# Optimization experiments

Measured on AMD Instinct MI355X. Metric: run time of the kernel, lower is better.

Reference implementation:

```python
import jax, jax.numpy as jnp
import numpy as np

B, L, D, H, A, NLAYERS, P = 16, 512, 768, 4, 100, 2, 3
DK = A // H  # 25
EPS = 1e-6


def setup_inputs() -> dict:
    key = jax.random.key(0)
    ks = jax.random.split(key, 20)
    s = 0.02
    return {
        "sequence_output": jax.random.normal(ks[0], (B, L, D), jnp.float32),
        "syntax_matrix": jax.random.normal(ks[1], (B, H, L, L), jnp.float32),
        # LayerNorm params
        "ln_a": jnp.ones((D,), jnp.float32),
        "ln_b": jnp.zeros((D,), jnp.float32),
        # Wxx: bert_dim -> attdim
        "Wxx_w": jax.random.normal(ks[2], (A, D), jnp.float32) * s,
        "Wxx_b": jnp.zeros((A,), jnp.float32),
        # attention q/k projections (attdim -> attdim)
        "q_w": jax.random.normal(ks[3], (A, A), jnp.float32) * s,
        "q_b": jnp.zeros((A,), jnp.float32),
        "k_w": jax.random.normal(ks[4], (A, A), jnp.float32) * s,
        "k_b": jnp.zeros((A,), jnp.float32),
        # W: attdim -> attdim
        "W_w": jax.random.normal(ks[5], (A, A), jnp.float32) * s,
        "W_b": jnp.zeros((A,), jnp.float32),
        # Wx: (H + 2*attdim) -> H
        "Wx_w": jax.random.normal(ks[6], (H, H + 2 * A), jnp.float32) * s,
        "Wx_b": jnp.zeros((H,), jnp.float32),
        # aggregate_W: attdim*(layers+1) -> attdim
        "agg_w": jax.random.normal(ks[7], (A, A * (NLAYERS + 1)), jnp.float32) * s,
        "agg_b": jnp.zeros((A,), jnp.float32),
        # classifier: 100 -> polarities_dim
        "cls_w": jax.random.normal(ks[8], (P, A), jnp.float32) * s,
        "cls_b": jnp.zeros((P,), jnp.float32),
        # masks (ints)
        "mask_ids": jnp.ones((B, L), jnp.int32),
        "src_mask": jnp.ones((B, L), jnp.int32),
    }


def reference(sequence_output, syntax_matrix, ln_a, ln_b, Wxx_w, Wxx_b,
              q_w, q_b, k_w, k_b, W_w, W_b, Wx_w, Wx_b,
              agg_w, agg_b, cls_w, cls_b, mask_ids, src_mask):
    # custom LayerNorm: torch.std is unbiased (ddof=1)
    mean = sequence_output.mean(-1, keepdims=True)
    std = jnp.std(sequence_output, axis=-1, ddof=1, keepdims=True)
    seq = ln_a * (sequence_output - mean) / (std + EPS) + ln_b

    # Wxx projection to attdim (dropout = identity in eval)
    x = seq @ Wxx_w.T + Wxx_b  # [B, L, A]

    # multi-head attention producing adjacency [B, H, L, L]
    q = (x @ q_w.T + q_b).reshape(B, L, H, DK).transpose(0, 2, 1, 3)
    k = (x @ k_w.T + k_b).reshape(B, L, H, DK).transpose(0, 2, 1, 3)
    scores = jnp.einsum('bhid,bhjd->bhij', q, k) / jnp.sqrt(jnp.float32(DK))
    key_mask = src_mask[:, None, None, :]  # [B,1,1,L]
    scores = jnp.where(key_mask == 0, jnp.float32(-1e9), scores)
    scores = scores + syntax_matrix
    adj = jax.nn.softmax(scores, axis=-1)  # [B, H, L, L]

    # split Wx into its adjacency / node-j / node-i blocks so the [B,L,L,H+2A]
    # concat tensor is never materialized (edge MLP is linear => decomposable)
    Aw = Wx_w[:, :H]            # [H, H]
    B1 = Wx_w[:, H:H + A]       # [H, A] applied to x[b, j]
    B2 = Wx_w[:, H + A:]        # [H, A] applied to x[b, i]

    x_g = x
    layer_list = [x]
    for i in range(NLAYERS):
        # Ax = mean over heads of adj_h @ x  (x identical per head)
        Ax = jnp.einsum('bhij,bjd->bid', adj, x_g) / H
        x_g = jax.nn.relu(Ax @ W_w.T + W_b)  # [B, L, A]
        layer_list.append(x_g)
        # edge update: edge[b,g,i,j] = sum_h Aw[g,h]*adj[b,h,i,j]
        e_adj = jnp.einsum('bhij,gh->bgij', adj, Aw)  # [B, H, L, L]
        u = jnp.einsum('bjd,gd->bgj', x_g, B1)        # node1 (index j)
        v = jnp.einsum('bid,gd->bgi', x_g, B2)        # node2 (index i)
        adj = e_adj + u[:, :, None, :] + v[:, :, :, None] + Wx_b[None, :, None, None]

    feats = jnp.concatenate(layer_list, axis=-1)          # [B, L, A*(NLAYERS+1)]
    node = jax.nn.relu(feats @ agg_w.T + agg_b)           # [B, L, A]

    valid_len = jnp.clip(mask_ids.sum(axis=1), 1, None).astype(node.dtype)[:, None]
    pooled = node.sum(axis=1) / valid_len                 # [B, A]
    logits = pooled @ cls_w.T + cls_b                     # [B, P]
    return logits
```

## Files before the change

### kernel.cpp

```cpp
#include <hip/hip_runtime.h>

#define B_ 16
#define L_ 512
#define D_ 768
#define H_ 4
#define A_ 100
#define DK_ 25
#define P_ 3
#define XP_ 128

__global__ __launch_bounds__(256) void k_prep(
    const float* __restrict__ Wxx_w, const float* __restrict__ agg_w,
    const float* __restrict__ q_w, const float* __restrict__ k_w,
    const float* __restrict__ W_w,
    float* __restrict__ wT, float* __restrict__ aggT,
    float* __restrict__ qkT, float* __restrict__ WT)
{
    int idx = blockIdx.x * 256 + threadIdx.x;
    if (idx < 98304) {
        const int d = idx >> 7, a = idx & 127;
        wT[idx] = (a < A_) ? Wxx_w[(size_t)a * D_ + d] : 0.f;
        return;
    }
    idx -= 98304;
    if (idx < 38400) {
        const int n = idx & 127, k = (idx >> 7) % A_, c = idx / (128 * A_);
        aggT[idx] = (n < A_) ? agg_w[(size_t)n * (3 * A_) + c * A_ + k] : 0.f;
        return;
    }
    idx -= 38400;
    if (idx < 25600) {
        const int n = idx & 255, k = idx >> 8;
        const int half = n >> 7, a = n & 127;
        const float* w = half ? k_w : q_w;
        qkT[idx] = (a < A_) ? w[(size_t)a * A_ + k] : 0.f;
        return;
    }
    idx -= 25600;
    if (idx < 12800) {
        const int n = idx & 127, k = idx >> 7;
        WT[idx] = (n < A_) ? W_w[(size_t)n * A_ + k] : 0.f;
    }
}

__global__ __launch_bounds__(256) void k_lnx(
    const float* __restrict__ seq, const float* __restrict__ ln_a, const float* __restrict__ ln_b,
    const float* __restrict__ wT, const float* __restrict__ Wxx_b, float* __restrict__ xp)
{
    __shared__ float ss[32][36];
    __shared__ float ws[32][128];
    __shared__ float mean_s[32], rd_s[32];
    const int tid = threadIdx.x;
    const int row0 = blockIdx.x * 32;
    const int wv = tid >> 6, lane = tid & 63;

    for (int rr = 0; rr < 8; ++rr) {
        const int r = wv * 8 + rr;
        const float4* src = (const float4*)(seq + (size_t)(row0 + r) * D_);
        float4 a = src[lane], b = src[lane + 64], c = src[lane + 128];
        float s = a.x + a.y + a.z + a.w + b.x + b.y + b.z + b.w + c.x + c.y + c.z + c.w;
        #pragma unroll
        for (int o = 32; o; o >>= 1) s += __shfl_xor(s, o);
        const float m = s * (1.0f / 768.0f);
        float q = (a.x-m)*(a.x-m) + (a.y-m)*(a.y-m) + (a.z-m)*(a.z-m) + (a.w-m)*(a.w-m)
                + (b.x-m)*(b.x-m) + (b.y-m)*(b.y-m) + (b.z-m)*(b.z-m) + (b.w-m)*(b.w-m)
                + (c.x-m)*(c.x-m) + (c.y-m)*(c.y-m) + (c.z-m)*(c.z-m) + (c.w-m)*(c.w-m);
        #pragma unroll
        for (int o = 32; o; o >>= 1) q += __shfl_xor(q, o);
        if (lane == 0) {
            mean_s[r] = m;
            rd_s[r] = 1.0f / (sqrtf(q * (1.0f / 767.0f)) + 1e-6f);
        }
    }
    __syncthreads();

    const int c4 = tid & 31, rg = tid >> 5;
    float4 acc[4];
    #pragma unroll
    for (int i = 0; i < 4; ++i) { acc[i].x = acc[i].y = acc[i].z = acc[i].w = 0.f; }

    for (int kc = 0; kc < 24; ++kc) {
        {
            const int r = tid >> 3, k4 = tid & 7;
            float4 v = *(const float4*)(seq + (size_t)(row0 + r) * D_ + kc * 32 + k4 * 4);
            float4 la = ((const float4*)ln_a)[kc * 8 + k4];
            float4 lb = ((const float4*)ln_b)[kc * 8 + k4];
            const float m = mean_s[r], rd = rd_s[r];
            float4 o;
            o.x = la.x * ((v.x - m) * rd) + lb.x;
            o.y = la.y * ((v.y - m) * rd) + lb.y;
            o.z = la.z * ((v.z - m) * rd) + lb.z;
            o.w = la.w * ((v.w - m) * rd) + lb.w;
            *(float4*)&ss[r][k4 * 4] = o;
        }
        #pragma unroll
        for (int t = 0; t < 4; ++t) {
            const int idx = tid + t * 256;
            const int k = idx >> 5, cc = idx & 31;
            *(float4*)&ws[k][cc * 4] = *(const float4*)(wT + (size_t)(kc * 32 + k) * 128 + cc * 4);
        }
        __syncthreads();
        #pragma unroll 2
        for (int k = 0; k < 32; k += 4) {
            float4 sv[4];
            #pragma unroll
            for (int i = 0; i < 4; ++i) sv[i] = *(float4*)&ss[rg * 4 + i][k];
            #pragma unroll
            for (int j = 0; j < 4; ++j) {
                float4 w4 = *(float4*)&ws[k + j][c4 * 4];
                #pragma unroll
                for (int i = 0; i < 4; ++i) {
                    const float sj = ((float*)&sv[i])[j];
                    acc[i].x += sj * w4.x; acc[i].y += sj * w4.y;
                    acc[i].z += sj * w4.z; acc[i].w += sj * w4.w;
                }
            }
        }
        __syncthreads();
    }

    float4 bias = {0.f, 0.f, 0.f, 0.f};
    if (c4 < 25) bias = ((const float4*)Wxx_b)[c4];
    #pragma unroll
    for (int i = 0; i < 4; ++i) {
        float4 o;
        o.x = acc[i].x + bias.x; o.y = acc[i].y + bias.y;
        o.z = acc[i].z + bias.z; o.w = acc[i].w + bias.w;
        *(float4*)(xp + (size_t)(row0 + rg * 4 + i) * XP_ + c4 * 4) = o;
    }
}

__global__ __launch_bounds__(256) void k_qkg(
    const float* __restrict__ xp, const float* __restrict__ qkT,
    const float* __restrict__ q_b, const float* __restrict__ k_b,
    float* __restrict__ qt, float* __restrict__ kt)
{
    __shared__ float ss[32][104];
    __shared__ float ws[A_][128];
    const int tid = threadIdx.x;
    const int row0 = blockIdx.x * 32;
    const int half = blockIdx.y;
    const int c4 = tid & 31, rg = tid >> 5;

    for (int idx = tid; idx < 32 * 25; idx += 256) {
        const int r = idx / 25, k4 = idx % 25;
        *(float4*)&ss[r][k4 * 4] = *(const float4*)(xp + (size_t)(row0 + r) * XP_ + k4 * 4);
    }
    for (int idx = tid; idx < A_ * 32; idx += 256) {
        const int k = idx >> 5, cc = idx & 31;
        *(float4*)&ws[k][cc * 4] = *(const float4*)(qkT + (size_t)k * 256 + half * 128 + cc * 4);
    }
    __syncthreads();

    float4 acc[4];
    #pragma unroll
    for (int i = 0; i < 4; ++i) { acc[i].x = acc[i].y = acc[i].z = acc[i].w = 0.f; }
    #pragma unroll 5
    for (int k = 0; k < A_; k += 4) {
        float4 sv[4];
        #pragma unroll
        for (int i = 0; i < 4; ++i) sv[i] = *(float4*)&ss[rg * 4 + i][k];
        #pragma unroll
        for (int j = 0; j < 4; ++j) {
            float4 w4 = *(float4*)&ws[k + j][c4 * 4];
            #pragma unroll
            for (int i = 0; i < 4; ++i) {
                const float sj = ((float*)&sv[i])[j];
                acc[i].x += sj * w4.x; acc[i].y += sj * w4.y;
                acc[i].z += sj * w4.z; acc[i].w += sj * w4.w;
            }
        }
    }

    if (c4 < 25) {
        const float4 bias = ((const float4*)(half ? k_b : q_b))[c4];
        float* dst = half ? kt : qt;
        #pragma unroll
        for (int i = 0; i < 4; ++i) {
            float4 o;
            o.x = acc[i].x + bias.x; o.y = acc[i].y + bias.y;
            o.z = acc[i].z + bias.z; o.w = acc[i].w + bias.w;
            *(float4*)(dst + (size_t)(row0 + rg * 4 + i) * A_ + c4 * 4) = o;
        }
    }
}

#define NI_ 8
#define SCS 516
__global__ __launch_bounds__(256) void k_attn(
    const float* __restrict__ qt, const float* __restrict__ kt,
    const float* __restrict__ syn, const int* __restrict__ src_mask,
    const float* __restrict__ Wx_w, float* __restrict__ es)
{
    __shared__ __align__(16) float sc[32 * SCS];
    __shared__ __align__(16) float qs[NI_ * 4 * 28];
    __shared__ float mrow[32], irow[32];
    __shared__ float cs[4];

    const int tid = threadIdx.x;
    const int b = blockIdx.y;
    const int i0 = blockIdx.x * NI_;
    const int wv = tid >> 6, lane = tid & 63;

    for (int idx = tid; idx < NI_ * 4 * 25; idx += 256) {
        const int i = idx / 100, rem = idx % 100;
        const int h = rem / 25, d = rem % 25;
        qs[(i * 4 + h) * 28 + d] = qt[(size_t)(b * L_ + i0 + i) * A_ + h * DK_ + d];
    }
    if (tid < 4) cs[tid] = Wx_w[tid] + Wx_w[204 + tid] + Wx_w[408 + tid] + Wx_w[612 + tid];
    __syncthreads();

    const float* q0b = qs + (size_t)(wv * 2 + 0) * 4 * 28;
    const float* q1b = qs + (size_t)(wv * 2 + 1) * 4 * 28;
    const int r0 = (wv * 2 + 0) * 4;
    const int r1 = (wv * 2 + 1) * 4;

    float mx[4][2];
    #pragma unroll
    for (int h = 0; h < 4; ++h) { mx[h][0] = -3.0e38f; mx[h][1] = -3.0e38f; }

    #pragma unroll 1
    for (int t = 0; t < 8; ++t) {
        const int j = t * 64 + lane;
        const float4* krp = (const float4*)(kt + (size_t)(b * L_ + j) * A_);
        float4 kv[25];
        #pragma unroll
        for (int c = 0; c < 25; ++c) kv[c] = krp[c];
        const int mk = src_mask[b * L_ + j];
        const float msc = mk ? 0.2f : 0.f;
        const float mbias = mk ? 0.f : -1e9f;
        #pragma unroll
        for (int h = 0; h < 4; ++h) {
            const float* qa_ = q0b + h * 28;
            const float* qb_ = q1b + h * 28;
            float a0 = 0.f, a1 = 0.f;
            #pragma unroll
            for (int d = 0; d < 25; ++d) {
                const int e = h * 25 + d;
                const float kk = ((const float*)&kv[e >> 2])[e & 3];
                a0 += qa_[d] * kk;
                a1 += qb_[d] * kk;
            }
            const size_t sy0 = ((size_t)(b * H_ + h) * L_ + i0 + wv * 2) * L_ + j;
            const float s0 = a0 * msc + mbias + syn[sy0];
            const float s1 = a1 * msc + mbias + syn[sy0 + L_];
            sc[(r0 + h) * SCS + j] = s0;
            sc[(r1 + h) * SCS + j] = s1;
            mx[h][0] = fmaxf(mx[h][0], s0);
            mx[h][1] = fmaxf(mx[h][1], s1);
        }
    }
    #pragma unroll
    for (int h = 0; h < 4; ++h)
        #pragma unroll
        for (int il = 0; il < 2; ++il) {
            float m = mx[h][il];
            #pragma unroll
            for (int o = 32; o; o >>= 1) m = fmaxf(m, __shfl_xor(m, o));
            if (lane == 0) mrow[(wv * 2 + il) * 4 + h] = m;
        }
    __syncthreads();

    {
        const int r = tid >> 3, sub = tid & 7;
        const float m = mrow[r];
        float* row = sc + r * SCS;
        float sum = 0.f;
        #pragma unroll 8
        for (int n = 0; n < 64; ++n) {
            const int j = sub + n * 8;
            const float E = __expf(row[j] - m);
            row[j] = E;
            sum += E;
        }
        sum += __shfl_xor(sum, 1);
        sum += __shfl_xor(sum, 2);
        sum += __shfl_xor(sum, 4);
        if (sub == 0) irow[r] = 1.0f / sum;
    }
    __syncthreads();

    const float c0 = cs[0], c1 = cs[1], c2 = cs[2], c3 = cs[3];
    #pragma unroll
    for (int n = 0; n < 16; ++n) {
        const int idx = tid + n * 256;
        const int i = idx >> 9, j = idx & 511;
        const float v0 = irow[i * 4 + 0], v1 = irow[i * 4 + 1];
        const float v2 = irow[i * 4 + 2], v3 = irow[i * 4 + 3];
        const float p0 = sc[(i * 4 + 0) * SCS + j] * v0;
        const float p1 = sc[(i * 4 + 1) * SCS + j] * v1;
        const float p2 = sc[(i * 4 + 2) * SCS + j] * v2;
        const float p3 = sc[(i * 4 + 3) * SCS + j] * v3;
        es[((size_t)(b * H_ + 0) * L_ + i0 + i) * L_ + j] = p0 + p1 + p2 + p3;
        es[((size_t)(b * H_ + 1) * L_ + i0 + i) * L_ + j] = c0 * p0 + c1 * p1 + c2 * p2 + c3 * p3;
    }
}

template<int LAYER2>
__global__ __launch_bounds__(256) void k_axg(
    const float* __restrict__ adj, const float* __restrict__ xp,
    const float* __restrict__ S, const float* __restrict__ T,
    const float* __restrict__ Vv, const float* __restrict__ Wx_b,
    float* __restrict__ axb)
{
    __shared__ float ss[32][36];
    __shared__ float ws[32][128];
    const int tid = threadIdx.x;
    const int row0 = blockIdx.x * 32;
    const int b = row0 >> 9, i0 = row0 & 511;
    const float* adjb = adj + (size_t)b * 4 * L_ * L_;
    const int c4 = tid & 31, rg = tid >> 5;
    float4 acc[4];
    #pragma unroll
    for (int i = 0; i < 4; ++i) { acc[i].x = acc[i].y = acc[i].z = acc[i].w = 0.f; }

    for (int kc = 0; kc < 16; ++kc) {
        {
            const int r = tid >> 3, q4 = tid & 7;
            *(float4*)&ss[r][q4 * 4] =
                *(const float4*)(adjb + (size_t)(i0 + r) * L_ + kc * 32 + q4 * 4);
        }
        #pragma unroll
        for (int t = 0; t < 4; ++t) {
            const int idx = tid + t * 256;
            const int k = idx >> 5, cc = idx & 31;
            *(float4*)&ws[k][cc * 4] =
                *(const float4*)(xp + ((size_t)b * L_ + kc * 32 + k) * XP_ + cc * 4);
        }
        __syncthreads();
        #pragma unroll 2
        for (int k = 0; k < 32; k += 4) {
            float4 sv[4];
            #pragma unroll
            for (int i = 0; i < 4; ++i) sv[i] = *(float4*)&ss[rg * 4 + i][k];
            #pragma unroll
            for (int j = 0; j < 4; ++j) {
                float4 w4 = *(float4*)&ws[k + j][c4 * 4];
                #pragma unroll
                for (int i = 0; i < 4; ++i) {
                    const float sj = ((float*)&sv[i])[j];
                    acc[i].x += sj * w4.x; acc[i].y += sj * w4.y;
                    acc[i].z += sj * w4.z; acc[i].w += sj * w4.w;
                }
            }
        }
        __syncthreads();
    }

    float wb = 0.f;
    float4 Sv = {0.f, 0.f, 0.f, 0.f}, Tv = {0.f, 0.f, 0.f, 0.f};
    if (LAYER2) {
        wb = Wx_b[0] + Wx_b[1] + Wx_b[2] + Wx_b[3];
        if (c4 < 25) {
            Sv = ((const float4*)(S + b * A_))[c4];
            Tv = ((const float4*)(T + b * A_))[c4];
        }
    }
    #pragma unroll
    for (int i = 0; i < 4; ++i) {
        const int grow = row0 + rg * 4 + i;
        const float vv = LAYER2 ? (Vv[grow] + wb) : 0.f;
        float4 o;
        o.x = (acc[i].x + Sv.x + vv * Tv.x) * 0.25f;
        o.y = (acc[i].y + Sv.y + vv * Tv.y) * 0.25f;
        o.z = (acc[i].z + Sv.z + vv * Tv.z) * 0.25f;
        o.w = (acc[i].w + Sv.w + vv * Tv.w) * 0.25f;
        *(float4*)(axb + (size_t)grow * XP_ + c4 * 4) = o;
    }
}

__global__ __launch_bounds__(256) void k_xw(
    const float* __restrict__ axb, const float* __restrict__ WT,
    const float* __restrict__ W_b, float* __restrict__ xout)
{
    __shared__ float ss[32][104];
    __shared__ float ws[A_][128];
    const int tid = threadIdx.x;
    const int row0 = blockIdx.x * 32;
    const int c4 = tid & 31, rg = tid >> 5;

    for (int idx = tid; idx < 32 * 25; idx += 256) {
        const int r = idx / 25, k4 = idx % 25;
        *(float4*)&ss[r][k4 * 4] = *(const float4*)(axb + (size_t)(row0 + r) * XP_ + k4 * 4);
    }
    for (int idx = tid; idx < A_ * 32; idx += 256) {
        const int k = idx >> 5, cc = idx & 31;
        *(float4*)&ws[k][cc * 4] = *(const float4*)(WT + (size_t)k * 128 + cc * 4);
    }
    __syncthreads();

    float4 acc[4];
    #pragma unroll
    for (int i = 0; i < 4; ++i) { acc[i].x = acc[i].y = acc[i].z = acc[i].w = 0.f; }
    #pragma unroll 5
    for (int k = 0; k < A_; k += 4) {
        float4 sv[4];
        #pragma unroll
        for (int i = 0; i < 4; ++i) sv[i] = *(float4*)&ss[rg * 4 + i][k];
        #pragma unroll
        for (int j = 0; j < 4; ++j) {
            float4 w4 = *(float4*)&ws[k + j][c4 * 4];
            #pragma unroll
            for (int i = 0; i < 4; ++i) {
                const float sj = ((float*)&sv[i])[j];
                acc[i].x += sj * w4.x; acc[i].y += sj * w4.y;
                acc[i].z += sj * w4.z; acc[i].w += sj * w4.w;
            }
        }
    }

    float4 bias = {0.f, 0.f, 0.f, 0.f};
    if (c4 < 25) bias = ((const float4*)W_b)[c4];
    #pragma unroll
    for (int i = 0; i < 4; ++i) {
        float4 o;
        o.x = fmaxf(acc[i].x + bias.x, 0.f); o.y = fmaxf(acc[i].y + bias.y, 0.f);
        o.z = fmaxf(acc[i].z + bias.z, 0.f); o.w = fmaxf(acc[i].w + bias.w, 0.f);
        *(float4*)(xout + (size_t)(row0 + rg * 4 + i) * XP_ + c4 * 4) = o;
    }
}

__global__ __launch_bounds__(256) void k_extras(
    const float* __restrict__ x1, const float* __restrict__ Wx_w,
    float* __restrict__ Vv, float* __restrict__ T, float* __restrict__ S,
    float* __restrict__ pooled)
{
    __shared__ float b1s[A_], b2s[A_], Ul[L_];
    const int tid = threadIdx.x, b = blockIdx.x;
    if (tid < A_) {
        float s1 = 0.f, s2 = 0.f;
        #pragma unroll
        for (int g = 0; g < H_; ++g) {
            s1 += Wx_w[g * 204 + 4 + tid];
            s2 += Wx_w[g * 204 + 104 + tid];
        }
        b1s[tid] = s1; b2s[tid] = s2;
        pooled[b * A_ + tid] = 0.f;
    }
    __syncthreads();
    for (int j = tid; j < L_; j += 256) {
        const float* xr = x1 + ((size_t)b * L_ + j) * XP_;
        float u = 0.f, v = 0.f;
        #pragma unroll 4
        for (int c = 0; c < A_; ++c) { float xv = xr[c]; u += xv * b1s[c]; v += xv * b2s[c]; }
        Ul[j] = u;
        Vv[b * L_ + j] = v;
    }
    __syncthreads();
    if (tid < A_) {
        float t = 0.f, s = 0.f;
        for (int j = 0; j < L_; ++j) {
            float xv = x1[((size_t)b * L_ + j) * XP_ + tid];
            t += xv; s += Ul[j] * xv;
        }
        T[b * A_ + tid] = t; S[b * A_ + tid] = s;
    }
}

__global__ __launch_bounds__(256) void k_nodepool(
    const float* __restrict__ x, const float* __restrict__ x1, const float* __restrict__ x2,
    const float* __restrict__ aggT, const float* __restrict__ agg_b,
    float* __restrict__ pooled)
{
    __shared__ float ss[32][104];
    __shared__ float ws[A_][128];
    const int tid = threadIdx.x;
    const int row0 = blockIdx.x * 32;
    const int b = row0 >> 9;
    const int c4 = tid & 31, rg = tid >> 5;
    float4 acc[4];
    #pragma unroll
    for (int i = 0; i < 4; ++i) { acc[i].x = acc[i].y = acc[i].z = acc[i].w = 0.f; }

    for (int c = 0; c < 3; ++c) {
        const float* src = (c == 0) ? x : (c == 1) ? x1 : x2;
        for (int idx = tid; idx < 32 * 25; idx += 256) {
            const int r = idx / 25, k4 = idx % 25;
            *(float4*)&ss[r][k4 * 4] =
                *(const float4*)(src + (size_t)(row0 + r) * XP_ + k4 * 4);
        }
        for (int idx = tid; idx < A_ * 32; idx += 256) {
            const int k = idx >> 5, cc = idx & 31;
            *(float4*)&ws[k][cc * 4] =
                *(const float4*)(aggT + ((size_t)c * A_ + k) * 128 + cc * 4);
        }
        __syncthreads();
        #pragma unroll 5
        for (int k = 0; k < A_; k += 4) {
            float4 sv[4];
            #pragma unroll
            for (int i = 0; i < 4; ++i) sv[i] = *(float4*)&ss[rg * 4 + i][k];
            #pragma unroll
            for (int j = 0; j < 4; ++j) {
                float4 w4 = *(float4*)&ws[k + j][c4 * 4];
                #pragma unroll
                for (int i = 0; i < 4; ++i) {
                    const float sj = ((float*)&sv[i])[j];
                    acc[i].x += sj * w4.x; acc[i].y += sj * w4.y;
                    acc[i].z += sj * w4.z; acc[i].w += sj * w4.w;
                }
            }
        }
        __syncthreads();
    }

    float4 bias = {0.f, 0.f, 0.f, 0.f};
    if (c4 < 25) bias = ((const float4*)agg_b)[c4];
    float4 rs = {0.f, 0.f, 0.f, 0.f};
    #pragma unroll
    for (int i = 0; i < 4; ++i) {
        rs.x += fmaxf(acc[i].x + bias.x, 0.f);
        rs.y += fmaxf(acc[i].y + bias.y, 0.f);
        rs.z += fmaxf(acc[i].z + bias.z, 0.f);
        rs.w += fmaxf(acc[i].w + bias.w, 0.f);
    }
    float* red = &ss[0][0];
    __syncthreads();
    *(float4*)&red[rg * 128 + c4 * 4] = rs;
    __syncthreads();
    if (rg == 0 && c4 < 25) {
        float4 tot = {0.f, 0.f, 0.f, 0.f};
        #pragma unroll
        for (int g = 0; g < 8; ++g) {
            float4 v = *(float4*)&red[g * 128 + c4 * 4];
            tot.x += v.x; tot.y += v.y; tot.z += v.z; tot.w += v.w;
        }
        atomicAdd(&pooled[b * A_ + c4 * 4 + 0], tot.x);
        atomicAdd(&pooled[b * A_ + c4 * 4 + 1], tot.y);
        atomicAdd(&pooled[b * A_ + c4 * 4 + 2], tot.z);
        atomicAdd(&pooled[b * A_ + c4 * 4 + 3], tot.w);
    }
}

__global__ __launch_bounds__(64) void k_logits(
    const float* __restrict__ pooled, const float* __restrict__ cls_w,
    const float* __restrict__ cls_b, const int* __restrict__ mask_ids,
    float* __restrict__ out)
{
    const int tid = threadIdx.x;
    if (tid < B_ * P_) {
        const int b = tid / P_, p = tid % P_;
        int vs = 0;
        for (int l = 0; l < L_; ++l) vs += mask_ids[b * L_ + l];
        float inv = 1.0f / (float)max(vs, 1);
        float acc = cls_b[p];
        #pragma unroll 4
        for (int a = 0; a < A_; ++a) acc += (pooled[b * A_ + a] * inv) * cls_w[p * A_ + a];
        out[b * P_ + p] = acc;
    }
}

extern "C" void kernel_launch(void* const* d_in, const int* in_sizes, int n_in,
                              void* d_out, int out_size, void* d_ws, size_t ws_size,
                              hipStream_t stream) {
    const float* seq    = (const float*)d_in[0];
    const float* syn    = (const float*)d_in[1];
    const float* ln_a   = (const float*)d_in[2];
    const float* ln_b   = (const float*)d_in[3];
    const float* Wxx_w  = (const float*)d_in[4];
    const float* Wxx_b  = (const float*)d_in[5];
    const float* q_w    = (const float*)d_in[6];
    const float* q_b    = (const float*)d_in[7];
    const float* k_w    = (const float*)d_in[8];
    const float* k_b    = (const float*)d_in[9];
    const float* W_w    = (const float*)d_in[10];
    const float* W_b    = (const float*)d_in[11];
    const float* Wx_w   = (const float*)d_in[12];
    const float* Wx_b   = (const float*)d_in[13];
    const float* agg_w  = (const float*)d_in[14];
    const float* agg_b  = (const float*)d_in[15];
    const float* cls_w  = (const float*)d_in[16];
    const float* cls_b  = (const float*)d_in[17];
    const int* mask_ids = (const int*)d_in[18];
    const int* src_mask = (const int*)d_in[19];
    float* out = (float*)d_out;

    float* ws = (float*)d_ws;
    size_t off = 0;
    float* xp     = ws + off; off += (size_t)B_ * L_ * XP_;
    float* x1p    = ws + off; off += (size_t)B_ * L_ * XP_;
    float* x2p    = ws + off; off += (size_t)B_ * L_ * XP_;
    float* axb    = ws + off; off += (size_t)B_ * L_ * XP_;
    float* qt     = ws + off; off += (size_t)B_ * L_ * A_;
    float* kt     = ws + off; off += (size_t)B_ * L_ * A_;
    float* es     = ws + off; off += (size_t)B_ * H_ * L_ * L_;
    float* Vv     = ws + off; off += (size_t)B_ * L_;
    float* T      = ws + off; off += (size_t)B_ * A_;
    float* S      = ws + off; off += (size_t)B_ * A_;
    float* pooled = ws + off; off += (size_t)B_ * A_;
    float* wT     = ws + off; off += (size_t)D_ * 128;
    float* aggT   = ws + off; off += (size_t)3 * A_ * 128;
    float* qkT    = ws + off; off += (size_t)A_ * 256;
    float* WT     = ws + off; off += (size_t)A_ * 128;

    k_prep<<<(98304 + 38400 + 25600 + 12800 + 255) / 256, 256, 0, stream>>>(
        Wxx_w, agg_w, q_w, k_w, W_w, wT, aggT, qkT, WT);
    k_lnx<<<(B_ * L_) / 32, 256, 0, stream>>>(seq, ln_a, ln_b, wT, Wxx_b, xp);
    k_qkg<<<dim3((B_ * L_) / 32, 2), 256, 0, stream>>>(xp, qkT, q_b, k_b, qt, kt);
    k_attn<<<dim3(L_ / NI_, B_), 256, 0, stream>>>(qt, kt, syn, src_mask, Wx_w, es);
    k_axg<0><<<(B_ * L_) / 32, 256, 0, stream>>>(es, xp, nullptr, nullptr, nullptr, nullptr, axb);
    k_xw<<<(B_ * L_) / 32, 256, 0, stream>>>(axb, WT, W_b, x1p);
    k_extras<<<B_, 256, 0, stream>>>(x1p, Wx_w, Vv, T, S, pooled);
    k_axg<1><<<(B_ * L_) / 32, 256, 0, stream>>>(es + (size_t)L_ * L_, x1p, S, T, Vv, Wx_b, axb);
    k_xw<<<(B_ * L_) / 32, 256, 0, stream>>>(axb, WT, W_b, x2p);
    k_nodepool<<<(B_ * L_) / 32, 256, 0, stream>>>(xp, x1p, x2p, aggT, agg_b, pooled);
    k_logits<<<1, 64, 0, stream>>>(pooled, cls_w, cls_b, mask_ids, out);
}
```

Before: 441.8 us.

## Use head-major K layout and recompute scores with online softmax in attention

K is now written in a head-major, float4-per-position layout so each lane loads coalesced float4 vectors per head instead of an entire 100-float row. The attention kernel drops the 66KB shared score buffer and its syncs, running an online (running max/sum) softmax in a first pass and recomputing scores in a second pass to write the combined adjacency. This removes the large LDS footprint, which should raise occupancy. In exchange it reads syntax_matrix and K twice and does extra exp work.

```diff
diff --git a/kernel.cpp b/kernel.cpp
--- a/kernel.cpp
+++ b/kernel.cpp
@@ -133,7 +133,7 @@
 __global__ __launch_bounds__(256) void k_qkg(
     const float* __restrict__ xp, const float* __restrict__ qkT,
     const float* __restrict__ q_b, const float* __restrict__ k_b,
-    float* __restrict__ qt, float* __restrict__ kt)
+    float* __restrict__ qt, float* __restrict__ kt4)
 {
     __shared__ float ss[32][104];
     __shared__ float ws[A_][128];
@@ -173,28 +173,41 @@
     }
 
     if (c4 < 25) {
-        const float4 bias = ((const float4*)(half ? k_b : q_b))[c4];
-        float* dst = half ? kt : qt;
-        #pragma unroll
-        for (int i = 0; i < 4; ++i) {
-            float4 o;
-            o.x = acc[i].x + bias.x; o.y = acc[i].y + bias.y;
-            o.z = acc[i].z + bias.z; o.w = acc[i].w + bias.w;
-            *(float4*)(dst + (size_t)(row0 + rg * 4 + i) * A_ + c4 * 4) = o;
+        if (!half) {
+            const float4 bias = ((const float4*)q_b)[c4];
+            #pragma unroll
+            for (int i = 0; i < 4; ++i) {
+                float4 o;
+                o.x = acc[i].x + bias.x; o.y = acc[i].y + bias.y;
+                o.z = acc[i].z + bias.z; o.w = acc[i].w + bias.w;
+                *(float4*)(qt + (size_t)(row0 + rg * 4 + i) * A_ + c4 * 4) = o;
+            }
+        } else {
+            const float4 bias = ((const float4*)k_b)[c4];
+            const int bb = row0 >> 9;
+            const int jb = (row0 & 511) + rg * 4;
+            #pragma unroll
+            for (int cc = 0; cc < 4; ++cc) {
+                const int a = c4 * 4 + cc;
+                const int h = a / 25, dd = a % 25;
+                const int d4 = dd >> 2, sl = dd & 3;
+                const float bc = ((const float*)&bias)[cc];
+                float* dst = kt4 + ((((size_t)(bb * 4 + h) * 7 + d4) * 512) + jb) * 4 + sl;
+                #pragma unroll
+                for (int i = 0; i < 4; ++i)
+                    dst[i * 4] = ((const float*)&acc[i])[cc] + bc;
+            }
         }
     }
 }
 
 #define NI_ 8
-#define SCS 516
 __global__ __launch_bounds__(256) void k_attn(
-    const float* __restrict__ qt, const float* __restrict__ kt,
+    const float* __restrict__ qt, const float* __restrict__ kt4,
     const float* __restrict__ syn, const int* __restrict__ src_mask,
     const float* __restrict__ Wx_w, float* __restrict__ es)
 {
-    __shared__ __align__(16) float sc[32 * SCS];
     __shared__ __align__(16) float qs[NI_ * 4 * 28];
-    __shared__ float mrow[32], irow[32];
     __shared__ float cs[4];
 
     const int tid = threadIdx.x;
@@ -212,87 +225,102 @@
 
     const float* q0b = qs + (size_t)(wv * 2 + 0) * 4 * 28;
     const float* q1b = qs + (size_t)(wv * 2 + 1) * 4 * 28;
-    const int r0 = (wv * 2 + 0) * 4;
-    const int r1 = (wv * 2 + 1) * 4;
-
-    float mx[4][2];
-    #pragma unroll
-    for (int h = 0; h < 4; ++h) { mx[h][0] = -3.0e38f; mx[h][1] = -3.0e38f; }
-
-    #pragma unroll 1
+    const int ig0 = i0 + wv * 2;
+    const float4* ktb = (const float4*)kt4 + (size_t)(b * 4) * 7 * 512;
+
+    float mrun[4][2], srun[4][2];
+    #pragma unroll
+    for (int h = 0; h < 4; ++h)
+        #pragma unroll
+        for (int il = 0; il < 2; ++il) { mrun[h][il] = -3.0e38f; srun[h][il] = 0.f; }
+
+    #pragma unroll 2
     for (int t = 0; t < 8; ++t) {
         const int j = t * 64 + lane;
-        const float4* krp = (const float4*)(kt + (size_t)(b * L_ + j) * A_);
-        float4 kv[25];
-        #pragma unroll
-        for (int c = 0; c < 25; ++c) kv[c] = krp[c];
         const int mk = src_mask[b * L_ + j];
         const float msc = mk ? 0.2f : 0.f;
         const float mbias = mk ? 0.f : -1e9f;
         #pragma unroll
         for (int h = 0; h < 4; ++h) {
+            const float4* kp = ktb + (size_t)h * 7 * 512 + j;
             const float* qa_ = q0b + h * 28;
             const float* qb_ = q1b + h * 28;
             float a0 = 0.f, a1 = 0.f;
             #pragma unroll
-            for (int d = 0; d < 25; ++d) {
-                const int e = h * 25 + d;
-                const float kk = ((const float*)&kv[e >> 2])[e & 3];
-                a0 += qa_[d] * kk;
-                a1 += qb_[d] * kk;
-            }
-            const size_t sy0 = ((size_t)(b * H_ + h) * L_ + i0 + wv * 2) * L_ + j;
-            const float s0 = a0 * msc + mbias + syn[sy0];
-            const float s1 = a1 * msc + mbias + syn[sy0 + L_];
-            sc[(r0 + h) * SCS + j] = s0;
-            sc[(r1 + h) * SCS + j] = s1;
-            mx[h][0] = fmaxf(mx[h][0], s0);
-            mx[h][1] = fmaxf(mx[h][1], s1);
-        }
-    }
+            for (int d4 = 0; d4 < 6; ++d4) {
+                const float4 kk = kp[d4 * 512];
+                a0 += qa_[d4*4+0]*kk.x + qa_[d4*4+1]*kk.y + qa_[d4*4+2]*kk.z + qa_[d4*4+3]*kk.w;
+                a1 += qb_[d4*4+0]*kk.x + qb_[d4*4+1]*kk.y + qb_[d4*4+2]*kk.z + qb_[d4*4+3]*kk.w;
+            }
+            { const float4 kk = kp[6 * 512]; a0 += qa_[24] * kk.x; a1 += qb_[24] * kk.x; }
+            const size_t syb = ((size_t)(b * H_ + h) * L_ + ig0) * L_ + j;
+            const float s0 = a0 * msc + mbias + syn[syb];
+            const float s1 = a1 * msc + mbias + syn[syb + L_];
+            {
+                const float mo = mrun[h][0], mn = fmaxf(mo, s0);
+                srun[h][0] = srun[h][0] * __expf(mo - mn) + __expf(s0 - mn);
+                mrun[h][0] = mn;
+            }
+            {
+                const float mo = mrun[h][1], mn = fmaxf(mo, s1);
+                srun[h][1] = srun[h][1] * __expf(mo - mn) + __expf(s1 - mn);
+                mrun[h][1] = mn;
+            }
+        }
+    }
+
     #pragma unroll
     for (int h = 0; h < 4; ++h)
         #pragma unroll
         for (int il = 0; il < 2; ++il) {
-            float m = mx[h][il];
-            #pragma unroll
-            for (int o = 32; o; o >>= 1) m = fmaxf(m, __shfl_xor(m, o));
-            if (lane == 0) mrow[(wv * 2 + il) * 4 + h] = m;
-        }
-    __syncthreads();
-
-    {
-        const int r = tid >> 3, sub = tid & 7;
-        const float m = mrow[r];
-        float* row = sc + r * SCS;
-        float sum = 0.f;
-        #pragma unroll 8
-        for (int n = 0; n < 64; ++n) {
-            const int j = sub + n * 8;
-            const float E = __expf(row[j] - m);
-            row[j] = E;
-            sum += E;
-        }
-        sum += __shfl_xor(sum, 1);
-        sum += __shfl_xor(sum, 2);
-        sum += __shfl_xor(sum, 4);
-        if (sub == 0) irow[r] = 1.0f / sum;
-    }
-    __syncthreads();
+            float m = mrun[h][il], su = srun[h][il];
+            #pragma unroll
+            for (int o = 32; o; o >>= 1) {
+                const float mo = __shfl_xor(m, o);
+                const float so = __shfl_xor(su, o);
+                const float mn = fmaxf(m, mo);
+                su = su * __expf(m - mn) + so * __expf(mo - mn);
+                m = mn;
+            }
+            mrun[h][il] = m;
+            srun[h][il] = 1.0f / su;
+        }
 
     const float c0 = cs[0], c1 = cs[1], c2 = cs[2], c3 = cs[3];
-    #pragma unroll
-    for (int n = 0; n < 16; ++n) {
-        const int idx = tid + n * 256;
-        const int i = idx >> 9, j = idx & 511;
-        const float v0 = irow[i * 4 + 0], v1 = irow[i * 4 + 1];
-        const float v2 = irow[i * 4 + 2], v3 = irow[i * 4 + 3];
-        const float p0 = sc[(i * 4 + 0) * SCS + j] * v0;
-        const float p1 = sc[(i * 4 + 1) * SCS + j] * v1;
-        const float p2 = sc[(i * 4 + 2) * SCS + j] * v2;
-        const float p3 = sc[(i * 4 + 3) * SCS + j] * v3;
-        es[((size_t)(b * H_ + 0) * L_ + i0 + i) * L_ + j] = p0 + p1 + p2 + p3;
-        es[((size_t)(b * H_ + 1) * L_ + i0 + i) * L_ + j] = c0 * p0 + c1 * p1 + c2 * p2 + c3 * p3;
+
+    #pragma unroll 2
+    for (int t = 0; t < 8; ++t) {
+        const int j = t * 64 + lane;
+        const int mk = src_mask[b * L_ + j];
+        const float msc = mk ? 0.2f : 0.f;
+        const float mbias = mk ? 0.f : -1e9f;
+        float e00 = 0.f, e10 = 0.f, e01 = 0.f, e11 = 0.f;
+        #pragma unroll
+        for (int h = 0; h < 4; ++h) {
+            const float4* kp = ktb + (size_t)h * 7 * 512 + j;
+            const float* qa_ = q0b + h * 28;
+            const float* qb_ = q1b + h * 28;
+            float a0 = 0.f, a1 = 0.f;
+            #pragma unroll
+            for (int d4 = 0; d4 < 6; ++d4) {
+                const float4 kk = kp[d4 * 512];
+                a0 += qa_[d4*4+0]*kk.x + qa_[d4*4+1]*kk.y + qa_[d4*4+2]*kk.z + qa_[d4*4+3]*kk.w;
+                a1 += qb_[d4*4+0]*kk.x + qb_[d4*4+1]*kk.y + qb_[d4*4+2]*kk.z + qb_[d4*4+3]*kk.w;
+            }
+            { const float4 kk = kp[6 * 512]; a0 += qa_[24] * kk.x; a1 += qb_[24] * kk.x; }
+            const size_t syb = ((size_t)(b * H_ + h) * L_ + ig0) * L_ + j;
+            const float s0 = a0 * msc + mbias + syn[syb];
+            const float s1 = a1 * msc + mbias + syn[syb + L_];
+            const float p0 = __expf(s0 - mrun[h][0]) * srun[h][0];
+            const float p1 = __expf(s1 - mrun[h][1]) * srun[h][1];
+            const float ch = (h == 0) ? c0 : (h == 1) ? c1 : (h == 2) ? c2 : c3;
+            e00 += p0; e10 += ch * p0;
+            e01 += p1; e11 += ch * p1;
+        }
+        es[((size_t)(b * H_ + 0) * L_ + ig0) * L_ + j] = e00;
+        es[((size_t)(b * H_ + 1) * L_ + ig0) * L_ + j] = e10;
+        es[((size_t)(b * H_ + 0) * L_ + ig0 + 1) * L_ + j] = e01;
+        es[((size_t)(b * H_ + 1) * L_ + ig0 + 1) * L_ + j] = e11;
     }
 }
 
@@ -582,7 +610,7 @@
     float* x2p    = ws + off; off += (size_t)B_ * L_ * XP_;
     float* axb    = ws + off; off += (size_t)B_ * L_ * XP_;
     float* qt     = ws + off; off += (size_t)B_ * L_ * A_;
-    float* kt     = ws + off; off += (size_t)B_ * L_ * A_;
+    float* kt4    = ws + off; off += (size_t)B_ * 4 * 7 * L_ * 4;
     float* es     = ws + off; off += (size_t)B_ * H_ * L_ * L_;
     float* Vv     = ws + off; off += (size_t)B_ * L_;
     float* T      = ws + off; off += (size_t)B_ * A_;
@@ -596,8 +624,8 @@
     k_prep<<<(98304 + 38400 + 25600 + 12800 + 255) / 256, 256, 0, stream>>>(
         Wxx_w, agg_w, q_w, k_w, W_w, wT, aggT, qkT, WT);
     k_lnx<<<(B_ * L_) / 32, 256, 0, stream>>>(seq, ln_a, ln_b, wT, Wxx_b, xp);
-    k_qkg<<<dim3((B_ * L_) / 32, 2), 256, 0, stream>>>(xp, qkT, q_b, k_b, qt, kt);
-    k_attn<<<dim3(L_ / NI_, B_), 256, 0, stream>>>(qt, kt, syn, src_mask, Wx_w, es);
+    k_qkg<<<dim3((B_ * L_) / 32, 2), 256, 0, stream>>>(xp, qkT, q_b, k_b, qt, kt4);
+    k_attn<<<dim3(L_ / NI_, B_), 256, 0, stream>>>(qt, kt4, syn, src_mask, Wx_w, es);
     k_axg<0><<<(B_ * L_) / 32, 256, 0, stream>>>(es, xp, nullptr, nullptr, nullptr, nullptr, axb);
     k_xw<<<(B_ * L_) / 32, 256, 0, stream>>>(axb, WT, W_b, x1p);
     k_extras<<<B_, 256, 0, stream>>>(x1p, Wx_w, Vv, T, S, pooled);
```

Measured after the change: 765.7 us. 73.3% more time.

## Split fused attention into tiled score GEMM and separate row softmax kernel

Applied to the files above, without the earlier changes.

Replaces the single attention kernel, which held 32 score rows in shared memory, with a tiled 64x64 QK^T kernel that adds the syntax matrix and writes all four heads' scores to global memory. A second per-row kernel then does the softmax and the head combination. The aim is to improve occupancy and reuse through register tiling instead of per-lane dot products with high shared-memory use. The cost is an extra global round trip for the full score tensor.

```diff
diff --git a/kernel.cpp b/kernel.cpp
--- a/kernel.cpp
+++ b/kernel.cpp
@@ -185,114 +185,114 @@
     }
 }
 
-#define NI_ 8
-#define SCS 516
-__global__ __launch_bounds__(256) void k_attn(
+__global__ __launch_bounds__(256) void k_sgemm(
     const float* __restrict__ qt, const float* __restrict__ kt,
     const float* __restrict__ syn, const int* __restrict__ src_mask,
+    float* __restrict__ es)
+{
+    __shared__ float qs[DK_][64];
+    __shared__ float ks[DK_][64];
+    __shared__ int ms[64];
+    const int tid = threadIdx.x;
+    const int bh = blockIdx.z;
+    const int b = bh >> 2, h = bh & 3;
+    const int i0 = blockIdx.x * 64, j0 = blockIdx.y * 64;
+    const float* qbase = qt + ((size_t)b * L_ + i0) * A_ + h * DK_;
+    const float* kbase = kt + ((size_t)b * L_ + j0) * A_ + h * DK_;
+    {
+        const int r = tid >> 2, c = tid & 3;
+        #pragma unroll
+        for (int k = 0; k < 7; ++k) {
+            const int d = c + 4 * k;
+            if (d < DK_) {
+                qs[d][r] = qbase[(size_t)r * A_ + d];
+                ks[d][r] = kbase[(size_t)r * A_ + d];
+            }
+        }
+        if (tid < 64) ms[tid] = src_mask[b * L_ + j0 + tid];
+    }
+    __syncthreads();
+    const int ty = tid >> 4, tx = tid & 15;
+    float acc[4][4] = {};
+    #pragma unroll 5
+    for (int d = 0; d < DK_; ++d) {
+        float4 qv = *(const float4*)&qs[d][ty * 4];
+        float4 kv = *(const float4*)&ks[d][tx * 4];
+        const float q[4] = {qv.x, qv.y, qv.z, qv.w};
+        const float kk[4] = {kv.x, kv.y, kv.z, kv.w};
+        #pragma unroll
+        for (int ii = 0; ii < 4; ++ii)
+            #pragma unroll
+            for (int jj = 0; jj < 4; ++jj)
+                acc[ii][jj] += q[ii] * kk[jj];
+    }
+    const int irow = i0 + ty * 4, jcol = j0 + tx * 4;
+    const int m0 = ms[tx * 4], m1 = ms[tx * 4 + 1], m2 = ms[tx * 4 + 2], m3 = ms[tx * 4 + 3];
+    #pragma unroll
+    for (int ii = 0; ii < 4; ++ii) {
+        const size_t o = ((size_t)bh * L_ + irow + ii) * L_ + jcol;
+        float4 sv = *(const float4*)(syn + o);
+        float4 w;
+        w.x = (m0 ? acc[ii][0] * 0.2f : -1e9f) + sv.x;
+        w.y = (m1 ? acc[ii][1] * 0.2f : -1e9f) + sv.y;
+        w.z = (m2 ? acc[ii][2] * 0.2f : -1e9f) + sv.z;
+        w.w = (m3 ? acc[ii][3] * 0.2f : -1e9f) + sv.w;
+        *(float4*)(es + o) = w;
+    }
+}
+
+__global__ __launch_bounds__(256) void k_softmax(
     const float* __restrict__ Wx_w, float* __restrict__ es)
 {
-    __shared__ __align__(16) float sc[32 * SCS];
-    __shared__ __align__(16) float qs[NI_ * 4 * 28];
-    __shared__ float mrow[32], irow[32];
-    __shared__ float cs[4];
-
-    const int tid = threadIdx.x;
-    const int b = blockIdx.y;
-    const int i0 = blockIdx.x * NI_;
-    const int wv = tid >> 6, lane = tid & 63;
-
-    for (int idx = tid; idx < NI_ * 4 * 25; idx += 256) {
-        const int i = idx / 100, rem = idx % 100;
-        const int h = rem / 25, d = rem % 25;
-        qs[(i * 4 + h) * 28 + d] = qt[(size_t)(b * L_ + i0 + i) * A_ + h * DK_ + d];
-    }
-    if (tid < 4) cs[tid] = Wx_w[tid] + Wx_w[204 + tid] + Wx_w[408 + tid] + Wx_w[612 + tid];
-    __syncthreads();
-
-    const float* q0b = qs + (size_t)(wv * 2 + 0) * 4 * 28;
-    const float* q1b = qs + (size_t)(wv * 2 + 1) * 4 * 28;
-    const int r0 = (wv * 2 + 0) * 4;
-    const int r1 = (wv * 2 + 1) * 4;
-
-    float mx[4][2];
-    #pragma unroll
-    for (int h = 0; h < 4; ++h) { mx[h][0] = -3.0e38f; mx[h][1] = -3.0e38f; }
-
-    #pragma unroll 1
-    for (int t = 0; t < 8; ++t) {
-        const int j = t * 64 + lane;
-        const float4* krp = (const float4*)(kt + (size_t)(b * L_ + j) * A_);
-        float4 kv[25];
-        #pragma unroll
-        for (int c = 0; c < 25; ++c) kv[c] = krp[c];
-        const int mk = src_mask[b * L_ + j];
-        const float msc = mk ? 0.2f : 0.f;
-        const float mbias = mk ? 0.f : -1e9f;
-        #pragma unroll
-        for (int h = 0; h < 4; ++h) {
-            const float* qa_ = q0b + h * 28;
-            const float* qb_ = q1b + h * 28;
-            float a0 = 0.f, a1 = 0.f;
-            #pragma unroll
-            for (int d = 0; d < 25; ++d) {
-                const int e = h * 25 + d;
-                const float kk = ((const float*)&kv[e >> 2])[e & 3];
-                a0 += qa_[d] * kk;
-                a1 += qb_[d] * kk;
-            }
-            const size_t sy0 = ((size_t)(b * H_ + h) * L_ + i0 + wv * 2) * L_ + j;
-            const float s0 = a0 * msc + mbias + syn[sy0];
-            const float s1 = a1 * msc + mbias + syn[sy0 + L_];
-            sc[(r0 + h) * SCS + j] = s0;
-            sc[(r1 + h) * SCS + j] = s1;
-            mx[h][0] = fmaxf(mx[h][0], s0);
-            mx[h][1] = fmaxf(mx[h][1], s1);
-        }
-    }
-    #pragma unroll
-    for (int h = 0; h < 4; ++h)
-        #pragma unroll
-        for (int il = 0; il < 2; ++il) {
-            float m = mx[h][il];
-            #pragma unroll
-            for (int o = 32; o; o >>= 1) m = fmaxf(m, __shfl_xor(m, o));
-            if (lane == 0) mrow[(wv * 2 + il) * 4 + h] = m;
-        }
-    __syncthreads();
-
-    {
-        const int r = tid >> 3, sub = tid & 7;
-        const float m = mrow[r];
-        float* row = sc + r * SCS;
-        float sum = 0.f;
-        #pragma unroll 8
-        for (int n = 0; n < 64; ++n) {
-            const int j = sub + n * 8;
-            const float E = __expf(row[j] - m);
-            row[j] = E;
-            sum += E;
-        }
-        sum += __shfl_xor(sum, 1);
-        sum += __shfl_xor(sum, 2);
-        sum += __shfl_xor(sum, 4);
-        if (sub == 0) irow[r] = 1.0f / sum;
-    }
-    __syncthreads();
-
-    const float c0 = cs[0], c1 = cs[1], c2 = cs[2], c3 = cs[3];
-    #pragma unroll
-    for (int n = 0; n < 16; ++n) {
-        const int idx = tid + n * 256;
-        const int i = idx >> 9, j = idx & 511;
-        const float v0 = irow[i * 4 + 0], v1 = irow[i * 4 + 1];
-        const float v2 = irow[i * 4 + 2], v3 = irow[i * 4 + 3];
-        const float p0 = sc[(i * 4 + 0) * SCS + j] * v0;
-        const float p1 = sc[(i * 4 + 1) * SCS + j] * v1;
-        const float p2 = sc[(i * 4 + 2) * SCS + j] * v2;
-        const float p3 = sc[(i * 4 + 3) * SCS + j] * v3;
-        es[((size_t)(b * H_ + 0) * L_ + i0 + i) * L_ + j] = p0 + p1 + p2 + p3;
-        es[((size_t)(b * H_ + 1) * L_ + i0 + i) * L_ + j] = c0 * p0 + c1 * p1 + c2 * p2 + c3 * p3;
+    __shared__ float ps[H_][L_];
+    __shared__ float cs[H_];
+    const int tid = threadIdx.x, r = blockIdx.x;
+    const int b = r >> 9, i = r & 511;
+    const int h = tid >> 6, lane = tid & 63;
+    if (tid < H_) cs[tid] = Wx_w[tid] + Wx_w[204 + tid] + Wx_w[408 + tid] + Wx_w[612 + tid];
+    float* row = es + (((size_t)(b * H_ + h)) * L_ + i) * L_;
+    float4 v0 = ((const float4*)row)[lane];
+    float4 v1 = ((const float4*)row)[lane + 64];
+    float mx = fmaxf(fmaxf(fmaxf(v0.x, v0.y), fmaxf(v0.z, v0.w)),
+                     fmaxf(fmaxf(v1.x, v1.y), fmaxf(v1.z, v1.w)));
+    #pragma unroll
+    for (int o = 32; o; o >>= 1) mx = fmaxf(mx, __shfl_xor(mx, o));
+    float4 e0, e1;
+    e0.x = __expf(v0.x - mx); e0.y = __expf(v0.y - mx);
+    e0.z = __expf(v0.z - mx); e0.w = __expf(v0.w - mx);
+    e1.x = __expf(v1.x - mx); e1.y = __expf(v1.y - mx);
+    e1.z = __expf(v1.z - mx); e1.w = __expf(v1.w - mx);
+    float sum = e0.x + e0.y + e0.z + e0.w + e1.x + e1.y + e1.z + e1.w;
+    #pragma unroll
+    for (int o = 32; o; o >>= 1) sum += __shfl_xor(sum, o);
+    const float inv = 1.0f / sum;
+    e0.x *= inv; e0.y *= inv; e0.z *= inv; e0.w *= inv;
+    e1.x *= inv; e1.y *= inv; e1.z *= inv; e1.w *= inv;
+    *(float4*)&ps[h][lane * 4] = e0;
+    *(float4*)&ps[h][(lane + 64) * 4] = e1;
+    __syncthreads();
+    float* arow = es + (((size_t)(b * H_ + 0)) * L_ + i) * L_;
+    float* wrow = es + (((size_t)(b * H_ + 1)) * L_ + i) * L_;
+    const int t = tid & 127;
+    float4 p0 = *(float4*)&ps[0][t * 4];
+    float4 p1 = *(float4*)&ps[1][t * 4];
+    float4 p2 = *(float4*)&ps[2][t * 4];
+    float4 p3 = *(float4*)&ps[3][t * 4];
+    if (tid < 128) {
+        float4 o;
+        o.x = p0.x + p1.x + p2.x + p3.x;
+        o.y = p0.y + p1.y + p2.y + p3.y;
+        o.z = p0.z + p1.z + p2.z + p3.z;
+        o.w = p0.w + p1.w + p2.w + p3.w;
+        *(float4*)(arow + t * 4) = o;
+    } else {
+        const float c0 = cs[0], c1 = cs[1], c2 = cs[2], c3 = cs[3];
+        float4 o;
+        o.x = c0 * p0.x + c1 * p1.x + c2 * p2.x + c3 * p3.x;
+        o.y = c0 * p0.y + c1 * p1.y + c2 * p2.y + c3 * p3.y;
+        o.z = c0 * p0.z + c1 * p1.z + c2 * p2.z + c3 * p3.z;
+        o.w = c0 * p0.w + c1 * p1.w + c2 * p2.w + c3 * p3.w;
+        *(float4*)(wrow + t * 4) = o;
     }
 }
 
@@ -597,7 +597,8 @@
         Wxx_w, agg_w, q_w, k_w, W_w, wT, aggT, qkT, WT);
     k_lnx<<<(B_ * L_) / 32, 256, 0, stream>>>(seq, ln_a, ln_b, wT, Wxx_b, xp);
     k_qkg<<<dim3((B_ * L_) / 32, 2), 256, 0, stream>>>(xp, qkT, q_b, k_b, qt, kt);
-    k_attn<<<dim3(L_ / NI_, B_), 256, 0, stream>>>(qt, kt, syn, src_mask, Wx_w, es);
+    k_sgemm<<<dim3(8, 8, B_ * H_), 256, 0, stream>>>(qt, kt, syn, src_mask, es);
+    k_softmax<<<B_ * L_, 256, 0, stream>>>(Wx_w, es);
     k_axg<0><<<(B_ * L_) / 32, 256, 0, stream>>>(es, xp, nullptr, nullptr, nullptr, nullptr, axb);
     k_xw<<<(B_ * L_) / 32, 256, 0, stream>>>(axb, WT, W_b, x1p);
     k_extras<<<B_, 256, 0, stream>>>(x1p, Wx_w, Vv, T, S, pooled);
```

Result: faster. 384.2 us (-13.0%).
